# Performance work log

Hardware: AMD Instinct MI355X
Metric: run time of the kernel (lower is better)

The kernel has to match this reference:

```python
import jax, jax.numpy as jnp
import numpy as np

NC = 151  # number of object classes (VG)
NR = 51   # number of relation classes (VG)


def setup_inputs() -> dict:
    key = jax.random.key(0)
    ks = jax.random.split(key, 10)
    B, N, D = 32, 100, 4096
    H = D // 4
    w = lambda k, shape, fan_in: (jax.random.normal(k, shape, jnp.float32) / np.sqrt(fan_in).astype(np.float32))
    return {
        "encoder_reps": jax.random.normal(ks[0], (B * N, D), jnp.float32),
        "W_comp": w(ks[1], (D, H), D),        # obj_comp Linear (no bias)
        "W_ou1": w(ks[2], (H, H), H),         # ou1 Linear
        "W_ofc": w(ks[3], (H, H), H),         # ofc_u Linear
        "W_decomp": w(ks[4], (H, D), H),      # obj_decomp Linear
        "conv1": w(ks[5], (10, NR, 3, 3), NR * 9),  # Conv2d(51,10,3,pad=1)
        "conv2": w(ks[6], (5, 10, 3, 3), 10 * 9),   # Conv2d(10,5,3,pad=1)
        "conv3": w(ks[7], (1, 5, 1, 1), 5),         # Conv2d(5,1,1)
        "freq_emb": jax.random.normal(ks[8], (NC * NC, NR), jnp.float32) * 0.01,
        "obj_preds": jax.random.randint(ks[9], (B * N,), 0, NC),
        "num_obj": 100,
    }


def reference(encoder_reps, W_comp, W_ou1, W_ofc, W_decomp, conv1, conv2, conv3, freq_emb, obj_preds, num_obj):
    T, D = encoder_reps.shape
    N = num_obj
    B = T // N
    relu = jax.nn.relu
    # obj_comp then per-image ou1 (vectorized over images)
    comp = relu(encoder_reps @ W_comp).reshape(B, N, -1)   # [B,N,H]
    obj_u1 = relu(comp @ W_ou1)                             # [B,N,H]
    # product-index frequency-bias gather: emb[subj*NC + obj]
    labels = obj_preds.reshape(B, N)
    pair_idx = labels[:, :, None] * NC + labels[:, None, :]  # [B,N,N]
    adj_fg = freq_emb[pair_idx]                               # [B,N,N,NR]
    # adjacency net: Conv-Conv-Conv-Tanh over the NxN 'image' with NR channels
    x = jnp.transpose(adj_fg, (0, 3, 1, 2))                   # [B,NR,N,N]
    dn = ("NCHW", "OIHW", "NCHW")
    x = jax.lax.conv_general_dilated(x, conv1, (1, 1), "SAME", dimension_numbers=dn)
    x = jax.lax.conv_general_dilated(x, conv2, (1, 1), "SAME", dimension_numbers=dn)
    x = jnp.tanh(jax.lax.conv_general_dilated(x, conv3, (1, 1), "SAME", dimension_numbers=dn))
    adj = x[:, 0]                                             # [B,N,N]
    # graph message passing: adj @ obj_u1, then ofc_u / decomp + residual
    ofl_u = jnp.einsum("bnm,bmh->bnh", adj, obj_u1).reshape(T, -1)
    u_m = relu(ofl_u @ W_ofc)
    decomp = relu(u_m @ W_decomp)
    return decomp + encoder_reps
```

## Files before the change

kernel.cpp:

```cpp
#include <hip/hip_runtime.h>
#include <cmath>

#define NCC 151
#define NRCH 51
#define BDIM 32
#define NOBJ 100
#define DDIM 4096
#define HDIM 1024
#define TDIM (BDIM * NOBJ)

typedef __bf16 bf16_t;
typedef __bf16 bf16x8 __attribute__((ext_vector_type(8)));
typedef __bf16 bf16x4 __attribute__((ext_vector_type(4)));
typedef float f32x4 __attribute__((ext_vector_type(4)));

template <bool RELU, bool ADDF32OUT, int SPLITK, int MODE>
__global__ __launch_bounds__(256) void gemm_bf16(
    const bf16_t* __restrict__ A,
    const bf16_t* __restrict__ Bt,
    const float* __restrict__ add,
    void* __restrict__ Cout,
    int N, int K, size_t MN) {
  __shared__ __align__(16) bf16_t Asm[128 * 64];
  __shared__ __align__(16) bf16_t Bsm[128 * 64];
  const int tid = threadIdx.x;
  const int lane = tid & 63;
  const int w = tid >> 6;
  const int wm = w >> 1, wn = w & 1;

  const int nx = gridDim.x, ny = gridDim.y, nz = gridDim.z;
  const int h = blockIdx.x + nx * (blockIdx.y + ny * blockIdx.z);
  int bx, by, bz;
  if (MODE == 1) {
    bz = h & 7;
    const int s = h >> 3;
    by = s % ny;
    bx = s / ny;
  } else {
    const int nwg = nx * ny * nz;
    const int q = nwg >> 3;
    const int lin = (h & 7) * q + (h >> 3);
    by = lin % ny;
    const int r = lin / ny;
    bx = r % nx;
    bz = r / nx;
  }

  const int bm = by * 128, bn = bx * 128;
  const int lr = lane & 15;
  const int lk = lane >> 4;

  int kBeg = 0, kEnd = K;
  if (SPLITK > 1) {
    const int chunk = (((K / 64) + SPLITK - 1) / SPLITK) * 64;
    kBeg = bz * chunk;
    kEnd = min(K, kBeg + chunk);
  }

  f32x4 acc[4][4];
#pragma unroll
  for (int m = 0; m < 4; ++m)
#pragma unroll
    for (int n = 0; n < 4; ++n) acc[m][n] = (f32x4){0.f, 0.f, 0.f, 0.f};

  const int srow = tid >> 3;
  const int sslot = tid & 7;

  char* ldsA = (char*)Asm;
  char* ldsB = (char*)Bsm;

  for (int kt = kBeg; kt < kEnd; kt += 64) {
    __syncthreads();
#pragma unroll
    for (int i = 0; i < 4; ++i) {
      const int row = i * 32 + srow;
      const int kc = sslot ^ (row & 7);
      const bf16_t* ga = A + (size_t)(bm + row) * K + kt + kc * 8;
      const bf16_t* gb = Bt + (size_t)(bn + row) * K + kt + kc * 8;
      __builtin_amdgcn_global_load_lds(
          (const __attribute__((address_space(1))) void*)ga,
          (__attribute__((address_space(3))) void*)(ldsA + i * 4096 + w * 1024),
          16, 0, 0);
      __builtin_amdgcn_global_load_lds(
          (const __attribute__((address_space(1))) void*)gb,
          (__attribute__((address_space(3))) void*)(ldsB + i * 4096 + w * 1024),
          16, 0, 0);
    }
    __syncthreads();

    bf16x8 af[4][2], bfr[4][2];
#pragma unroll
    for (int m = 0; m < 4; ++m) {
      const int row = wm * 64 + m * 16 + lr;
#pragma unroll
      for (int kk = 0; kk < 2; ++kk) {
        const int slot = kk * 4 + lk;
        af[m][kk] =
            *(const bf16x8*)(ldsA + row * 128 + ((slot ^ (lr & 7)) << 4));
      }
    }
#pragma unroll
    for (int n = 0; n < 4; ++n) {
      const int row = wn * 64 + n * 16 + lr;
#pragma unroll
      for (int kk = 0; kk < 2; ++kk) {
        const int slot = kk * 4 + lk;
        bfr[n][kk] =
            *(const bf16x8*)(ldsB + row * 128 + ((slot ^ (lr & 7)) << 4));
      }
    }
#pragma unroll
    for (int m = 0; m < 4; ++m)
#pragma unroll
      for (int n = 0; n < 4; ++n) {
        acc[m][n] = __builtin_amdgcn_mfma_f32_16x16x32_bf16(
            af[m][0], bfr[n][0], acc[m][n], 0, 0, 0);
        acc[m][n] = __builtin_amdgcn_mfma_f32_16x16x32_bf16(
            af[m][1], bfr[n][1], acc[m][n], 0, 0, 0);
      }
  }

  const int or0 = bm + wm * 64 + lk * 4;
  const int oc0 = bn + wn * 64 + lr;
#pragma unroll
  for (int m = 0; m < 4; ++m)
#pragma unroll
    for (int n = 0; n < 4; ++n)
#pragma unroll
      for (int r = 0; r < 4; ++r) {
        float v = acc[m][n][r];
        const size_t off = (size_t)(or0 + m * 16 + r) * N + (oc0 + n * 16);
        if (SPLITK > 1) {
          ((bf16_t*)Cout)[bz * MN + off] = (bf16_t)v;
        } else {
          if (RELU) v = fmaxf(v, 0.f);
          if (ADDF32OUT)
            ((float*)Cout)[off] = v + add[off];
          else
            ((bf16_t*)Cout)[off] = (bf16_t)v;
        }
      }
}

template <int NPART>
__global__ __launch_bounds__(256) void reduceN_kernel(
    const bf16_t* __restrict__ p, bf16_t* __restrict__ out, int n8,
    size_t MN) {
  int i = blockIdx.x * 256 + threadIdx.x;
  if (i >= n8) return;
  float s[8] = {};
#pragma unroll
  for (int z = 0; z < NPART; ++z) {
    bf16x8 v = *(const bf16x8*)(p + z * MN + (size_t)i * 8);
#pragma unroll
    for (int j = 0; j < 8; ++j) s[j] += (float)v[j];
  }
  bf16x8 o;
#pragma unroll
  for (int j = 0; j < 8; ++j) o[j] = (bf16_t)fmaxf(s[j], 0.f);
  *(bf16x8*)(out + (size_t)i * 8) = o;
}

__global__ __launch_bounds__(256) void cvt_bf16_kernel(
    const float* __restrict__ in, bf16_t* __restrict__ out, int n4) {
  int i = blockIdx.x * 256 + threadIdx.x;
  if (i >= n4) return;
  float4 v = ((const float4*)in)[i];
  bf16x4 o = {(bf16_t)v.x, (bf16_t)v.y, (bf16_t)v.z, (bf16_t)v.w};
  ((bf16x4*)out)[i] = o;
}

__global__ __launch_bounds__(256) void transT_kernel(
    const float* __restrict__ in, bf16_t* __restrict__ out, int K, int N) {
  __shared__ float t[32][33];
  const int n0 = blockIdx.x * 32, k0 = blockIdx.y * 32;
  const int tx = threadIdx.x & 31, ty = threadIdx.x >> 5;
#pragma unroll
  for (int i = 0; i < 4; ++i)
    t[ty + i * 8][tx] = in[(size_t)(k0 + ty + i * 8) * N + n0 + tx];
  __syncthreads();
#pragma unroll
  for (int i = 0; i < 4; ++i)
    out[(size_t)(n0 + ty + i * 8) * K + k0 + tx] = (bf16_t)t[tx][ty + i * 8];
}

__global__ __launch_bounds__(256) void prep_w1r_kernel(
    const float* __restrict__ w1, float* __restrict__ w1r) {
  int idx = blockIdx.x * 256 + threadIdx.x;
  if (idx >= NRCH * 90) return;
  int ci = idx / 90, r = idx % 90, k9 = r / 10, co = r % 10;
  w1r[idx] = w1[((co * NRCH + ci) * 3 + k9 / 3) * 3 + (k9 % 3)];
}

__global__ __launch_bounds__(128) void prep_w23_kernel(
    const float* __restrict__ w2, const float* __restrict__ w3,
    float* __restrict__ w23) {
  int t = threadIdx.x;
  if (t >= 90) return;
  int k9 = t / 10, c2 = t % 10;
  float acc = 0.f;
#pragma unroll
  for (int c3 = 0; c3 < 5; ++c3)
    acc += w3[c3] * w2[((c3 * 10 + c2) * 3 + k9 / 3) * 3 + (k9 % 3)];
  w23[t] = acc;
}

__global__ __launch_bounds__(256) void pidx_kernel(
    const int* __restrict__ preds, int* __restrict__ pidx) {
  int idx = blockIdx.x * 256 + threadIdx.x;
  if (idx >= BDIM * NOBJ * NOBJ) return;
  int j = idx % NOBJ;
  int i = (idx / NOBJ) % NOBJ;
  int b = idx / (NOBJ * NOBJ);
  pidx[idx] = preds[b * NOBJ + i] * NCC + preds[b * NOBJ + j];
}

__global__ __launch_bounds__(128) void femb1_kernel(
    const float* __restrict__ femb, const float* __restrict__ w1r,
    float* __restrict__ femb1) {
  __shared__ float row[NRCH];
  const int p = blockIdx.x;
  if (threadIdx.x < NRCH)
    row[threadIdx.x] = femb[(size_t)p * NRCH + threadIdx.x];
  __syncthreads();
  const int t = threadIdx.x;
  if (t >= 90) return;
  float acc = 0.f;
#pragma unroll
  for (int ci = 0; ci < NRCH; ++ci) acc += row[ci] * w1r[ci * 90 + t];
  femb1[((size_t)p * 9 + t / 10) * 12 + (t % 10)] = acc;
}

__global__ __launch_bounds__(256) void conv1g_kernel(
    const int* __restrict__ pidx, const float* __restrict__ femb1,
    float* __restrict__ x1) {
  int idx = blockIdx.x * 256 + threadIdx.x;
  if (idx >= BDIM * NOBJ * NOBJ) return;
  int j = idx % NOBJ;
  int i = (idx / NOBJ) % NOBJ;
  int b = idx / (NOBJ * NOBJ);
  f32x4 a0 = {0.f, 0.f, 0.f, 0.f}, a1 = a0, a2 = a0;
  const int* pb = pidx + b * NOBJ * NOBJ;
#pragma unroll
  for (int kh = 0; kh < 3; ++kh) {
    int ii = i + kh - 1;
    if (ii < 0 || ii >= NOBJ) continue;
#pragma unroll
    for (int kw = 0; kw < 3; ++kw) {
      int jj = j + kw - 1;
      if (jj < 0 || jj >= NOBJ) continue;
      int p = pb[ii * NOBJ + jj];
      const f32x4* f =
          (const f32x4*)(femb1 + ((size_t)p * 9 + kh * 3 + kw) * 12);
      a0 += f[0];
      a1 += f[1];
      a2 += f[2];
    }
  }
  f32x4* o = (f32x4*)(x1 + (size_t)idx * 12);
  o[0] = a0;
  o[1] = a1;
  o[2] = a2;
}

__global__ __launch_bounds__(256) void conv23_kernel(
    const float* __restrict__ x1, const float* __restrict__ w23,
    float* __restrict__ adj) {
  __shared__ float w[90];
  if (threadIdx.x < 90) w[threadIdx.x] = w23[threadIdx.x];
  __syncthreads();
  int idx = blockIdx.x * 256 + threadIdx.x;
  if (idx >= BDIM * NOBJ * NOBJ) return;
  int j = idx % NOBJ;
  int i = (idx / NOBJ) % NOBJ;
  int b = idx / (NOBJ * NOBJ);
  float acc = 0.f;
  const float* xb = x1 + (size_t)b * NOBJ * NOBJ * 12;
#pragma unroll
  for (int kh = 0; kh < 3; ++kh) {
    int ii = i + kh - 1;
    if (ii < 0 || ii >= NOBJ) continue;
#pragma unroll
    for (int kw = 0; kw < 3; ++kw) {
      int jj = j + kw - 1;
      if (jj < 0 || jj >= NOBJ) continue;
      const float* xr = xb + (ii * NOBJ + jj) * 12;
      const float* wr = w + (kh * 3 + kw) * 10;
#pragma unroll
      for (int c = 0; c < 10; ++c) acc += wr[c] * xr[c];
    }
  }
  adj[idx] = tanhf(acc);
}

__global__ __launch_bounds__(256) void einsum_mfma_kernel(
    const float* __restrict__ adj,
    const bf16_t* __restrict__ u1,
    bf16_t* __restrict__ ofl) {
  __shared__ __align__(16) bf16_t As[128 * 128];
  __shared__ __align__(16) bf16_t Us[128 * 128];
  const int b = blockIdx.y;
  const int h0 = blockIdx.x * 128;
  const int tid = threadIdx.x, lane = tid & 63, w = tid >> 6;
  const int wm = w >> 1, wn = w & 1;
  const int lr = lane & 15, lk = lane >> 4;

  {
    f32x4 z = {0.f, 0.f, 0.f, 0.f};
#pragma unroll
    for (int i = 0; i < 8; ++i) ((f32x4*)As)[tid + i * 256] = z;
#pragma unroll
    for (int i = 0; i < 8; ++i) ((f32x4*)Us)[tid + i * 256] = z;
  }
  __syncthreads();

  const float* ab = adj + (size_t)b * 10000;
#pragma unroll
  for (int i = 0; i < 10; ++i) {
    int idx = tid + i * 256;
    if (idx < 2500) {
      int row = idx / 25, kc = idx % 25;
      f32x4 v = ((const f32x4*)ab)[idx];
      bf16x4 o = {(bf16_t)v[0], (bf16_t)v[1], (bf16_t)v[2], (bf16_t)v[3]};
      int slot = kc >> 1;
      *(bf16x4*)((char*)As + row * 256 + ((slot ^ (row & 7)) << 4) +
                 (kc & 1) * 8) = o;
    }
  }

  const bf16_t* ub = u1 + (size_t)b * 100 * HDIM + h0;
#pragma unroll
  for (int i = 0; i < 7; ++i) {
    int idx = tid + i * 256;
    if (idx < 1600) {
      int hc = idx / 100, m = idx % 100;
      bf16x8 v = *(const bf16x8*)(ub + (size_t)m * HDIM + hc * 8);
      int slot = m >> 3, mr = m & 7;
#pragma unroll
      for (int j = 0; j < 8; ++j) {
        int h = hc * 8 + j;
        *((bf16_t*)((char*)Us + h * 256 + ((slot ^ (h & 7)) << 4) + mr * 2)) =
            v[j];
      }
    }
  }
  __syncthreads();

  f32x4 acc[4][4];
#pragma unroll
  for (int m = 0; m < 4; ++m)
#pragma unroll
    for (int n = 0; n < 4; ++n) acc[m][n] = (f32x4){0.f, 0.f, 0.f, 0.f};

#pragma unroll
  for (int ks = 0; ks < 4; ++ks) {
    bf16x8 a[4], u[4];
#pragma unroll
    for (int m = 0; m < 4; ++m) {
      int row = wm * 64 + m * 16 + lr;
      int slot = ks * 4 + lk;
      a[m] = *(const bf16x8*)((char*)As + row * 256 + ((slot ^ (lr & 7)) << 4));
    }
#pragma unroll
    for (int n = 0; n < 4; ++n) {
      int row = wn * 64 + n * 16 + lr;
      int slot = ks * 4 + lk;
      u[n] = *(const bf16x8*)((char*)Us + row * 256 + ((slot ^ (lr & 7)) << 4));
    }
#pragma unroll
    for (int m = 0; m < 4; ++m)
#pragma unroll
      for (int n = 0; n < 4; ++n)
        acc[m][n] = __builtin_amdgcn_mfma_f32_16x16x32_bf16(a[m], u[n],
                                                            acc[m][n], 0, 0, 0);
  }

  const int or0 = wm * 64 + lk * 4;
  const int oc0 = h0 + wn * 64 + lr;
#pragma unroll
  for (int m = 0; m < 4; ++m)
#pragma unroll
    for (int n = 0; n < 4; ++n)
#pragma unroll
      for (int r = 0; r < 4; ++r) {
        int row = or0 + m * 16 + r;
        if (row < 100)
          ofl[((size_t)b * 100 + row) * HDIM + oc0 + n * 16] =
              (bf16_t)acc[m][n][r];
      }
}

extern "C" void kernel_launch(void* const* d_in, const int* in_sizes, int n_in,
                              void* d_out, int out_size, void* d_ws,
                              size_t ws_size, hipStream_t stream) {
  const float* enc = (const float*)d_in[0];
  const float* W_comp = (const float*)d_in[1];
  const float* W_ou1 = (const float*)d_in[2];
  const float* W_ofc = (const float*)d_in[3];
  const float* W_dec = (const float*)d_in[4];
  const float* conv1w = (const float*)d_in[5];
  const float* conv2w = (const float*)d_in[6];
  const float* conv3w = (const float*)d_in[7];
  const float* femb = (const float*)d_in[8];
  const int* preds = (const int*)d_in[9];
  float* out = (float*)d_out;
  char* wsb = (char*)d_ws;

  const size_t MN = (size_t)TDIM * HDIM;

  bf16_t* encb   = (bf16_t*)(wsb + 0);
  bf16_t* WcompT = (bf16_t*)(wsb + 26214400);
  bf16_t* comp   = (bf16_t*)(wsb + 34603008);
  bf16_t* part8  = (bf16_t*)(wsb + 41156608);
  bf16_t* Wou1T  = (bf16_t*)(wsb + 41156608);
  bf16_t* part3a = (bf16_t*)(wsb + 43253760);
  bf16_t* part3b = (bf16_t*)(wsb + 43253760);
  float*  w1r    = (float*)(wsb + 43253760);
  float*  w23    = (float*)(wsb + 43272128);
  float*  femb1  = (float*)(wsb + 43272512);
  int*    pidx   = (int*)(wsb + 53122560);
  float*  x1     = (float*)(wsb + 54402560);
  bf16_t* obj_u1 = (bf16_t*)(wsb + 69762560);
  float*  adj    = (float*)(wsb + 76316160);
  bf16_t* ofl_u  = (bf16_t*)(wsb + 0);
  bf16_t* WofcT  = (bf16_t*)(wsb + 6553600);
  bf16_t* u_m    = (bf16_t*)(wsb + 8650752);
  bf16_t* WdecT  = (bf16_t*)(wsb + 15204352);

  const int n8 = (int)(MN / 8);

  cvt_bf16_kernel<<<(TDIM * DDIM / 4 + 255) / 256, 256, 0, stream>>>(
      enc, encb, TDIM * DDIM / 4);
  transT_kernel<<<dim3(HDIM / 32, DDIM / 32), 256, 0, stream>>>(
      W_comp, WcompT, DDIM, HDIM);

  gemm_bf16<false, false, 8, 1>
      <<<dim3(HDIM / 128, TDIM / 128, 8), 256, 0, stream>>>(
          encb, WcompT, nullptr, part8, HDIM, DDIM, MN);
  reduceN_kernel<8><<<n8 / 256, 256, 0, stream>>>(part8, comp, n8, MN);

  transT_kernel<<<dim3(HDIM / 32, HDIM / 32), 256, 0, stream>>>(
      W_ou1, Wou1T, HDIM, HDIM);
  gemm_bf16<false, false, 3, 0>
      <<<dim3(HDIM / 128, TDIM / 128, 3), 256, 0, stream>>>(
          comp, Wou1T, nullptr, part3a, HDIM, HDIM, MN);
  reduceN_kernel<3><<<n8 / 256, 256, 0, stream>>>(part3a, obj_u1, n8, MN);

  prep_w1r_kernel<<<(NRCH * 90 + 255) / 256, 256, 0, stream>>>(conv1w, w1r);
  prep_w23_kernel<<<1, 128, 0, stream>>>(conv2w, conv3w, w23);
  pidx_kernel<<<(BDIM * NOBJ * NOBJ + 255) / 256, 256, 0, stream>>>(preds,
                                                                    pidx);
  femb1_kernel<<<NCC * NCC, 128, 0, stream>>>(femb, w1r, femb1);

  conv1g_kernel<<<(BDIM * NOBJ * NOBJ + 255) / 256, 256, 0, stream>>>(
      pidx, femb1, x1);
  conv23_kernel<<<(BDIM * NOBJ * NOBJ + 255) / 256, 256, 0, stream>>>(x1, w23,
                                                                      adj);

  transT_kernel<<<dim3(HDIM / 32, HDIM / 32), 256, 0, stream>>>(
      W_ofc, WofcT, HDIM, HDIM);
  transT_kernel<<<dim3(DDIM / 32, HDIM / 32), 256, 0, stream>>>(
      W_dec, WdecT, HDIM, DDIM);

  einsum_mfma_kernel<<<dim3(HDIM / 128, BDIM), 256, 0, stream>>>(adj, obj_u1,
                                                                 ofl_u);

  gemm_bf16<false, false, 3, 0>
      <<<dim3(HDIM / 128, TDIM / 128, 3), 256, 0, stream>>>(
          ofl_u, WofcT, nullptr, part3b, HDIM, HDIM, MN);
  reduceN_kernel<3><<<n8 / 256, 256, 0, stream>>>(part3b, u_m, n8, MN);

  gemm_bf16<true, true, 1, 0>
      <<<dim3(DDIM / 128, TDIM / 128), 256, 0, stream>>>(
          u_m, WdecT, enc, out, DDIM, HDIM, MN);
}
```

Before: 253.5 us.

## Fold conv2/conv3 into a per-pair 5x5 table, drop split-K, use bf16 residual

Conv2 and conv3 are pre-composed with the conv1-projected frequency embedding into a per-class-pair 5x5 effective-kernel table. The adjacency is then a 25-tap gather, with explicit subtraction terms to correct the zero padding at the image border. This removes the 12-channel x1 intermediate write and read. The two 1024x1024 GEMMs now run without split-K and apply ReLU in the epilogue, which removes the reduce kernels but launches fewer blocks. The final residual add reads the bf16 copy of encoder_reps instead of fp32, which lowers traffic at the cost of residual precision.

```diff
diff --git a/kernel.cpp b/kernel.cpp
--- a/kernel.cpp
+++ b/kernel.cpp
@@ -14,11 +14,11 @@
 typedef __bf16 bf16x4 __attribute__((ext_vector_type(4)));
 typedef float f32x4 __attribute__((ext_vector_type(4)));
 
-template <bool RELU, bool ADDF32OUT, int SPLITK, int MODE>
+template <bool RELU, bool ADDBF16, int SPLITK, int MODE>
 __global__ __launch_bounds__(256) void gemm_bf16(
     const bf16_t* __restrict__ A,
     const bf16_t* __restrict__ Bt,
-    const float* __restrict__ add,
+    const bf16_t* __restrict__ add,
     void* __restrict__ Cout,
     int N, int K, size_t MN) {
   __shared__ __align__(16) bf16_t Asm[128 * 64];
@@ -134,8 +134,8 @@
           ((bf16_t*)Cout)[bz * MN + off] = (bf16_t)v;
         } else {
           if (RELU) v = fmaxf(v, 0.f);
-          if (ADDF32OUT)
-            ((float*)Cout)[off] = v + add[off];
+          if (ADDBF16)
+            ((float*)Cout)[off] = v + (float)add[off];
           else
             ((bf16_t*)Cout)[off] = (bf16_t)v;
         }
@@ -231,64 +231,78 @@
   femb1[((size_t)p * 9 + t / 10) * 12 + (t % 10)] = acc;
 }
 
-__global__ __launch_bounds__(256) void conv1g_kernel(
-    const int* __restrict__ pidx, const float* __restrict__ femb1,
-    float* __restrict__ x1) {
+__global__ __launch_bounds__(128) void femb2_kernel(
+    const float* __restrict__ femb1, const float* __restrict__ w23,
+    float* __restrict__ femb2, float* __restrict__ femb2s) {
+  __shared__ float f1[90];
+  __shared__ float w[90];
+  __shared__ float g[81];
+  const int p = blockIdx.x;
+  const int t = threadIdx.x;
+  if (t < 90) {
+    f1[t] = femb1[((size_t)p * 9 + t / 10) * 12 + (t % 10)];
+    w[t] = w23[t];
+  }
+  __syncthreads();
+  if (t < 81) {
+    int d2 = t / 9, d1 = t % 9;
+    float a = 0.f;
+#pragma unroll
+    for (int c = 0; c < 10; ++c) a += w[d2 * 10 + c] * f1[d1 * 10 + c];
+    g[t] = a;
+    femb2[(size_t)p * 81 + t] = a;
+  }
+  __syncthreads();
+  if (t < 25) {
+    int eh = t / 5 - 2, ew = t % 5 - 2;
+    float s = 0.f;
+#pragma unroll
+    for (int d2h = -1; d2h <= 1; ++d2h)
+#pragma unroll
+      for (int d2w = -1; d2w <= 1; ++d2w) {
+        int d1h = eh - d2h, d1w = ew - d2w;
+        if (d1h < -1 || d1h > 1 || d1w < -1 || d1w > 1) continue;
+        s += g[((d2h + 1) * 3 + d2w + 1) * 9 + (d1h + 1) * 3 + (d1w + 1)];
+      }
+    femb2s[(size_t)p * 25 + t] = s;
+  }
+}
+
+__global__ __launch_bounds__(256) void adj25_kernel(
+    const int* __restrict__ pidx, const float* __restrict__ f2s,
+    const float* __restrict__ f2, float* __restrict__ adj) {
   int idx = blockIdx.x * 256 + threadIdx.x;
   if (idx >= BDIM * NOBJ * NOBJ) return;
   int j = idx % NOBJ;
   int i = (idx / NOBJ) % NOBJ;
   int b = idx / (NOBJ * NOBJ);
-  f32x4 a0 = {0.f, 0.f, 0.f, 0.f}, a1 = a0, a2 = a0;
   const int* pb = pidx + b * NOBJ * NOBJ;
-#pragma unroll
-  for (int kh = 0; kh < 3; ++kh) {
-    int ii = i + kh - 1;
+  float acc = 0.f;
+#pragma unroll
+  for (int eh = -2; eh <= 2; ++eh) {
+    int ii = i + eh;
     if (ii < 0 || ii >= NOBJ) continue;
 #pragma unroll
-    for (int kw = 0; kw < 3; ++kw) {
-      int jj = j + kw - 1;
+    for (int ew = -2; ew <= 2; ++ew) {
+      int jj = j + ew;
       if (jj < 0 || jj >= NOBJ) continue;
-      int p = pb[ii * NOBJ + jj];
-      const f32x4* f =
-          (const f32x4*)(femb1 + ((size_t)p * 9 + kh * 3 + kw) * 12);
-      a0 += f[0];
-      a1 += f[1];
-      a2 += f[2];
-    }
-  }
-  f32x4* o = (f32x4*)(x1 + (size_t)idx * 12);
-  o[0] = a0;
-  o[1] = a1;
-  o[2] = a2;
-}
-
-__global__ __launch_bounds__(256) void conv23_kernel(
-    const float* __restrict__ x1, const float* __restrict__ w23,
-    float* __restrict__ adj) {
-  __shared__ float w[90];
-  if (threadIdx.x < 90) w[threadIdx.x] = w23[threadIdx.x];
-  __syncthreads();
-  int idx = blockIdx.x * 256 + threadIdx.x;
-  if (idx >= BDIM * NOBJ * NOBJ) return;
-  int j = idx % NOBJ;
-  int i = (idx / NOBJ) % NOBJ;
-  int b = idx / (NOBJ * NOBJ);
-  float acc = 0.f;
-  const float* xb = x1 + (size_t)b * NOBJ * NOBJ * 12;
-#pragma unroll
-  for (int kh = 0; kh < 3; ++kh) {
-    int ii = i + kh - 1;
-    if (ii < 0 || ii >= NOBJ) continue;
-#pragma unroll
-    for (int kw = 0; kw < 3; ++kw) {
-      int jj = j + kw - 1;
-      if (jj < 0 || jj >= NOBJ) continue;
-      const float* xr = xb + (ii * NOBJ + jj) * 12;
-      const float* wr = w + (kh * 3 + kw) * 10;
-#pragma unroll
-      for (int c = 0; c < 10; ++c) acc += wr[c] * xr[c];
-    }
+      acc += f2s[(size_t)pb[ii * NOBJ + jj] * 25 + (eh + 2) * 5 + (ew + 2)];
+    }
+  }
+  if (i < 1 || i > NOBJ - 2 || j < 1 || j > NOBJ - 2) {
+    for (int d2h = -1; d2h <= 1; ++d2h)
+      for (int d2w = -1; d2w <= 1; ++d2w) {
+        int qi = i + d2h, qj = j + d2w;
+        if (qi >= 0 && qi < NOBJ && qj >= 0 && qj < NOBJ) continue;
+        for (int d1h = -1; d1h <= 1; ++d1h)
+          for (int d1w = -1; d1w <= 1; ++d1w) {
+            int ti = qi + d1h, tj = qj + d1w;
+            if (ti < 0 || ti >= NOBJ || tj < 0 || tj >= NOBJ) continue;
+            acc -= f2[(size_t)pb[ti * NOBJ + tj] * 81 +
+                      ((d2h + 1) * 3 + d2w + 1) * 9 + (d1h + 1) * 3 +
+                      (d1w + 1)];
+          }
+      }
   }
   adj[idx] = tanhf(acc);
 }
@@ -413,19 +427,18 @@
   bf16_t* comp   = (bf16_t*)(wsb + 34603008);
   bf16_t* part8  = (bf16_t*)(wsb + 41156608);
   bf16_t* Wou1T  = (bf16_t*)(wsb + 41156608);
-  bf16_t* part3a = (bf16_t*)(wsb + 43253760);
-  bf16_t* part3b = (bf16_t*)(wsb + 43253760);
   float*  w1r    = (float*)(wsb + 43253760);
   float*  w23    = (float*)(wsb + 43272128);
   float*  femb1  = (float*)(wsb + 43272512);
   int*    pidx   = (int*)(wsb + 53122560);
-  float*  x1     = (float*)(wsb + 54402560);
+  float*  femb2  = (float*)(wsb + 54402560);
+  float*  femb2s = (float*)(wsb + 61790208);
   bf16_t* obj_u1 = (bf16_t*)(wsb + 69762560);
   float*  adj    = (float*)(wsb + 76316160);
-  bf16_t* ofl_u  = (bf16_t*)(wsb + 0);
-  bf16_t* WofcT  = (bf16_t*)(wsb + 6553600);
-  bf16_t* u_m    = (bf16_t*)(wsb + 8650752);
-  bf16_t* WdecT  = (bf16_t*)(wsb + 15204352);
+  bf16_t* ofl_u  = (bf16_t*)(wsb + 26214400);
+  bf16_t* WofcT  = (bf16_t*)(wsb + 32768000);
+  bf16_t* u_m    = (bf16_t*)(wsb + 34865152);
+  bf16_t* WdecT  = (bf16_t*)(wsb + 41418752);
 
   const int n8 = (int)(MN / 8);
 
@@ -441,21 +454,19 @@
 
   transT_kernel<<<dim3(HDIM / 32, HDIM / 32), 256, 0, stream>>>(
       W_ou1, Wou1T, HDIM, HDIM);
-  gemm_bf16<false, false, 3, 0>
-      <<<dim3(HDIM / 128, TDIM / 128, 3), 256, 0, stream>>>(
-          comp, Wou1T, nullptr, part3a, HDIM, HDIM, MN);
-  reduceN_kernel<3><<<n8 / 256, 256, 0, stream>>>(part3a, obj_u1, n8, MN);
+  gemm_bf16<true, false, 1, 0>
+      <<<dim3(HDIM / 128, TDIM / 128), 256, 0, stream>>>(
+          comp, Wou1T, nullptr, obj_u1, HDIM, HDIM, MN);
 
   prep_w1r_kernel<<<(NRCH * 90 + 255) / 256, 256, 0, stream>>>(conv1w, w1r);
   prep_w23_kernel<<<1, 128, 0, stream>>>(conv2w, conv3w, w23);
   pidx_kernel<<<(BDIM * NOBJ * NOBJ + 255) / 256, 256, 0, stream>>>(preds,
                                                                     pidx);
   femb1_kernel<<<NCC * NCC, 128, 0, stream>>>(femb, w1r, femb1);
-
-  conv1g_kernel<<<(BDIM * NOBJ * NOBJ + 255) / 256, 256, 0, stream>>>(
-      pidx, femb1, x1);
-  conv23_kernel<<<(BDIM * NOBJ * NOBJ + 255) / 256, 256, 0, stream>>>(x1, w23,
-                                                                      adj);
+  femb2_kernel<<<NCC * NCC, 128, 0, stream>>>(femb1, w23, femb2, femb2s);
+
+  adj25_kernel<<<(BDIM * NOBJ * NOBJ + 255) / 256, 256, 0, stream>>>(
+      pidx, femb2s, femb2, adj);
 
   transT_kernel<<<dim3(HDIM / 32, HDIM / 32), 256, 0, stream>>>(
       W_ofc, WofcT, HDIM, HDIM);
@@ -465,12 +476,11 @@
   einsum_mfma_kernel<<<dim3(HDIM / 128, BDIM), 256, 0, stream>>>(adj, obj_u1,
                                                                  ofl_u);
 
-  gemm_bf16<false, false, 3, 0>
-      <<<dim3(HDIM / 128, TDIM / 128, 3), 256, 0, stream>>>(
-          ofl_u, WofcT, nullptr, part3b, HDIM, HDIM, MN);
-  reduceN_kernel<3><<<n8 / 256, 256, 0, stream>>>(part3b, u_m, n8, MN);
+  gemm_bf16<true, false, 1, 0>
+      <<<dim3(HDIM / 128, TDIM / 128), 256, 0, stream>>>(
+          ofl_u, WofcT, nullptr, u_m, HDIM, HDIM, MN);
 
   gemm_bf16<true, true, 1, 0>
       <<<dim3(DDIM / 128, TDIM / 128), 256, 0, stream>>>(
-          u_m, WdecT, enc, out, DDIM, HDIM, MN);
-}
+          u_m, WdecT, encb, out, DDIM, HDIM, MN);
+}
```

Result: slower. 264.4 us (+4.3%).

## Rebalance split-K across XCDs, drop split-K for square GEMMs, read bf16 residual

Applied to the files above, without the earlier changes.

The first GEMM drops from 8-way to 4-way split-K. It uses a new block-to-XCD mapping (MODE 3) that hands each XCD pair a contiguous set of row tiles for one K-split, and surplus blocks exit early. The two 1024x1024 GEMMs no longer use split-K, so their ReLU is applied inside the GEMM epilogue and two reduction kernels and their partial-buffer traffic go away. The final residual add now reads the bf16 copy of the encoder activations instead of fp32, halving that read but adding rounding error to the residual path. Workspace offsets are moved so the bf16 activations stay alive until the end.

```diff
diff --git a/kernel.cpp b/kernel.cpp
--- a/kernel.cpp
+++ b/kernel.cpp
@@ -14,11 +14,11 @@
 typedef __bf16 bf16x4 __attribute__((ext_vector_type(4)));
 typedef float f32x4 __attribute__((ext_vector_type(4)));
 
-template <bool RELU, bool ADDF32OUT, int SPLITK, int MODE>
+template <bool RELU, bool ADDBF16, int SPLITK, int MODE>
 __global__ __launch_bounds__(256) void gemm_bf16(
     const bf16_t* __restrict__ A,
     const bf16_t* __restrict__ Bt,
-    const float* __restrict__ add,
+    const bf16_t* __restrict__ add,
     void* __restrict__ Cout,
     int N, int K, size_t MN) {
   __shared__ __align__(16) bf16_t Asm[128 * 64];
@@ -36,6 +36,25 @@
     const int s = h >> 3;
     by = s % ny;
     bx = s / ny;
+  } else if (MODE == 3) {
+    const int xcd = h & 7, s = h >> 3;
+    bz = xcd >> 1;
+    const int half = xcd & 1;
+    if (half == 1 && s >= 96) return;
+    const int c = s / 40;
+    if (c < 2) {
+      const int within = s % 40;
+      bx = within / 5;
+      by = (half ? 13 : 0) + c * 5 + within % 5;
+    } else if (half == 0) {
+      const int w2 = s - 80;
+      bx = w2 / 3;
+      by = 10 + w2 % 3;
+    } else {
+      const int w2 = s - 80;
+      bx = w2 / 2;
+      by = 23 + w2 % 2;
+    }
   } else {
     const int nwg = nx * ny * nz;
     const int q = nwg >> 3;
@@ -134,8 +153,8 @@
           ((bf16_t*)Cout)[bz * MN + off] = (bf16_t)v;
         } else {
           if (RELU) v = fmaxf(v, 0.f);
-          if (ADDF32OUT)
-            ((float*)Cout)[off] = v + add[off];
+          if (ADDBF16)
+            ((float*)Cout)[off] = v + (float)add[off];
           else
             ((bf16_t*)Cout)[off] = (bf16_t)v;
         }
@@ -411,10 +430,8 @@
   bf16_t* encb   = (bf16_t*)(wsb + 0);
   bf16_t* WcompT = (bf16_t*)(wsb + 26214400);
   bf16_t* comp   = (bf16_t*)(wsb + 34603008);
-  bf16_t* part8  = (bf16_t*)(wsb + 41156608);
+  bf16_t* part4  = (bf16_t*)(wsb + 41156608);
   bf16_t* Wou1T  = (bf16_t*)(wsb + 41156608);
-  bf16_t* part3a = (bf16_t*)(wsb + 43253760);
-  bf16_t* part3b = (bf16_t*)(wsb + 43253760);
   float*  w1r    = (float*)(wsb + 43253760);
   float*  w23    = (float*)(wsb + 43272128);
   float*  femb1  = (float*)(wsb + 43272512);
@@ -422,10 +439,10 @@
   float*  x1     = (float*)(wsb + 54402560);
   bf16_t* obj_u1 = (bf16_t*)(wsb + 69762560);
   float*  adj    = (float*)(wsb + 76316160);
-  bf16_t* ofl_u  = (bf16_t*)(wsb + 0);
-  bf16_t* WofcT  = (bf16_t*)(wsb + 6553600);
-  bf16_t* u_m    = (bf16_t*)(wsb + 8650752);
-  bf16_t* WdecT  = (bf16_t*)(wsb + 15204352);
+  bf16_t* ofl_u  = (bf16_t*)(wsb + 26214400);
+  bf16_t* WofcT  = (bf16_t*)(wsb + 32768000);
+  bf16_t* u_m    = (bf16_t*)(wsb + 34865152);
+  bf16_t* WdecT  = (bf16_t*)(wsb + 41418752);
 
   const int n8 = (int)(MN / 8);
 
@@ -434,17 +451,15 @@
   transT_kernel<<<dim3(HDIM / 32, DDIM / 32), 256, 0, stream>>>(
       W_comp, WcompT, DDIM, HDIM);
 
-  gemm_bf16<false, false, 8, 1>
-      <<<dim3(HDIM / 128, TDIM / 128, 8), 256, 0, stream>>>(
-          encb, WcompT, nullptr, part8, HDIM, DDIM, MN);
-  reduceN_kernel<8><<<n8 / 256, 256, 0, stream>>>(part8, comp, n8, MN);
+  gemm_bf16<false, false, 4, 3><<<dim3(832, 1, 1), 256, 0, stream>>>(
+      encb, WcompT, nullptr, part4, HDIM, DDIM, MN);
+  reduceN_kernel<4><<<n8 / 256, 256, 0, stream>>>(part4, comp, n8, MN);
 
   transT_kernel<<<dim3(HDIM / 32, HDIM / 32), 256, 0, stream>>>(
       W_ou1, Wou1T, HDIM, HDIM);
-  gemm_bf16<false, false, 3, 0>
-      <<<dim3(HDIM / 128, TDIM / 128, 3), 256, 0, stream>>>(
-          comp, Wou1T, nullptr, part3a, HDIM, HDIM, MN);
-  reduceN_kernel<3><<<n8 / 256, 256, 0, stream>>>(part3a, obj_u1, n8, MN);
+  gemm_bf16<true, false, 1, 0>
+      <<<dim3(HDIM / 128, TDIM / 128), 256, 0, stream>>>(
+          comp, Wou1T, nullptr, obj_u1, HDIM, HDIM, MN);
 
   prep_w1r_kernel<<<(NRCH * 90 + 255) / 256, 256, 0, stream>>>(conv1w, w1r);
   prep_w23_kernel<<<1, 128, 0, stream>>>(conv2w, conv3w, w23);
@@ -465,12 +480,11 @@
   einsum_mfma_kernel<<<dim3(HDIM / 128, BDIM), 256, 0, stream>>>(adj, obj_u1,
                                                                  ofl_u);
 
-  gemm_bf16<false, false, 3, 0>
-      <<<dim3(HDIM / 128, TDIM / 128, 3), 256, 0, stream>>>(
-          ofl_u, WofcT, nullptr, part3b, HDIM, HDIM, MN);
-  reduceN_kernel<3><<<n8 / 256, 256, 0, stream>>>(part3b, u_m, n8, MN);
+  gemm_bf16<true, false, 1, 0>
+      <<<dim3(HDIM / 128, TDIM / 128), 256, 0, stream>>>(
+          ofl_u, WofcT, nullptr, u_m, HDIM, HDIM, MN);
 
   gemm_bf16<true, true, 1, 0>
       <<<dim3(DDIM / 128, TDIM / 128), 256, 0, stream>>>(
-          u_m, WdecT, enc, out, DDIM, HDIM, MN);
-}
+          u_m, WdecT, encb, out, DDIM, HDIM, MN);
+}
```

New measurement: 249.2 us. No clear change (-1.7%).
